# Kernel optimization log

Hardware: AMD Instinct MI355X
Metric: run time of the kernel (lower is better)

## Reference

```python
import jax, jax.numpy as jnp
import numpy as np

IMG = 128; P = 16; ND = IMG // P; N = ND * ND  # 64 patches
INF = 3 * P * P      # 768 flattened patch features
ATT = 768; HID = 3072; OUT = 768; B = 64
EPS = 1e-5


def setup_inputs() -> dict:
    key = jax.random.key(0)
    ks = jax.random.split(key, 24)
    w = lambda k, shape: jax.random.normal(k, shape, jnp.float32) * 0.02
    return {
        "x": jax.random.normal(ks[0], (B, 3, IMG, IMG), jnp.float32),
        # per-patch q/k/v projections: [n, in, out] weights, [n, out] biases
        "Wq": w(ks[1], (N, INF, ATT)), "bq": w(ks[2], (N, ATT)),
        "Wk": w(ks[3], (N, INF, ATT)), "bk": w(ks[4], (N, ATT)),
        "Wv": w(ks[5], (N, INF, ATT)), "bv": w(ks[6], (N, ATT)),
        "ln_g": jnp.ones((ATT,), jnp.float32), "ln_b": jnp.zeros((ATT,), jnp.float32),
        "p1_w": w(ks[7], (INF, ATT)), "p1_b": w(ks[8], (ATT,)),
        "w0": w(ks[9], (ATT, HID)),  "b0": w(ks[10], (HID,)),
        "w1": w(ks[11], (HID, HID)), "b1": w(ks[12], (HID,)),
        "w2": w(ks[13], (HID, HID)), "b2": w(ks[14], (HID,)),
        "w3": w(ks[15], (HID, HID)), "b3": w(ks[16], (HID,)),
        "w4": w(ks[17], (HID, OUT)), "b4": w(ks[18], (OUT,)),
        "p2_w": w(ks[19], (ATT, OUT)), "p2_b": w(ks[20], (OUT,)),
    }


def _forward(x, Wq, bq, Wk, bk, Wv, bv, ln_g, ln_b, p1_w, p1_b,
             w0, b0, w1, b1, w2, b2, w3, b3, w4, b4, p2_w, p2_b):
    b_ = x.shape[0]
    # patch split (row-major over (i,j) blocks) then flatten channel*patch dims
    flat = x.reshape(b_, 3, ND, P, ND, P).transpose(0, 2, 4, 1, 3, 5).reshape(b_, N, INF)
    # per-patch projections, attention taken ACROSS the batch dim (as in source)
    q = jnp.einsum('bnf,nfd->bnd', flat, Wq) + bq
    k = jnp.einsum('bnf,nfd->bnd', flat, Wk) + bk
    v = jnp.einsum('bnf,nfd->bnd', flat, Wv) + bv
    scores = jnp.einsum('bnd,cnd->nbc', q, k) / jnp.sqrt(jnp.float32(ATT))  # [n,B,B]
    attn = jnp.einsum('nbc,cnd->bnd', jax.nn.softmax(scores, axis=-1), v)  # [B,n,ATT]
    # LayerNorm(att_features)
    mu = attn.mean(-1, keepdims=True)
    var = ((attn - mu) ** 2).mean(-1, keepdims=True)
    ln = (attn - mu) / jnp.sqrt(var + EPS) * ln_g + ln_b
    att = ln + flat @ p1_w + p1_b
    # linear stack (no nonlinearity in the source)
    h = att @ w0 + b0
    h = h @ w1 + b1
    h = h @ w2 + b2
    h = h @ w3 + b3
    h = h @ w4 + b4
    proj = h + att @ p2_w + p2_b
    return jax.nn.softmax(proj, axis=2)


def reference(x, Wq, bq, Wk, bk, Wv, bv, ln_g, ln_b, p1_w, p1_b,
              w0, b0, w1, b1, w2, b2, w3, b3, w4, b4, p2_w, p2_b):
    return _forward(x, Wq, bq, Wk, bk, Wv, bv, ln_g, ln_b, p1_w, p1_b,
                    w0, b0, w1, b1, w2, b2, w3, b3, w4, b4, p2_w, p2_b)
```

## Files before the change

kernel.cpp:

```cpp
#include <hip/hip_runtime.h>
#include <hip/hip_bf16.h>

using bf16 = __bf16;
using bf16x8 = __bf16 __attribute__((ext_vector_type(8)));
using f32x4 = float __attribute__((ext_vector_type(4)));

static constexpr long ROWEL = 64L * 768;

__device__ __forceinline__ void async16(void* lds, const void* g)
{
    __builtin_amdgcn_global_load_lds((const __attribute__((address_space(1))) void*)g,
                                     (__attribute__((address_space(3))) void*)lds, 16, 0, 0);
}

__global__ __launch_bounds__(256) void k_patchify(const float* __restrict__ x, bf16* __restrict__ flat)
{
    const int n = blockIdx.x;
    const int b = blockIdx.y;
    const int i_ = n >> 3, j_ = n & 7;
    for (int it = 0; it < 3; ++it) {
        int f = threadIdx.x + it * 256;
        int c = f >> 8, rem = f & 255, pi = rem >> 4, pj = rem & 15;
        float v = x[(((long)(b * 3 + c)) << 14) + ((i_ * 16 + pi) << 7) + (j_ * 16 + pj)];
        flat[(long)b * ROWEL + n * 768 + f] = (bf16)v;
    }
}

__global__ __launch_bounds__(256) void k_cvt_t(const float* __restrict__ W, bf16* __restrict__ Wt,
                                               int Kd, int Nd)
{
    __shared__ bf16 T[64 * 66];
    const int k0 = blockIdx.x * 64, n0 = blockIdx.y * 64;
    const int tid = threadIdx.x;
    const int kr = tid >> 4, nc = (tid & 15) * 4;
#pragma unroll
    for (int i = 0; i < 4; ++i) {
        f32x4 v = *(const f32x4*)(W + (long)(k0 + kr + i * 16) * Nd + n0 + nc);
#pragma unroll
        for (int e = 0; e < 4; ++e)
            T[(kr + i * 16) * 66 + nc + e] = (bf16)v[e];
    }
    __syncthreads();
    const int nr = tid >> 3, ks = (tid & 7) * 8;
#pragma unroll
    for (int it = 0; it < 2; ++it) {
        int n = nr + it * 32;
        bf16x8 o;
#pragma unroll
        for (int j = 0; j < 8; ++j) o[j] = T[(ks + j) * 66 + n];
        *(bf16x8*)(Wt + (long)(n0 + n) * Kd + k0 + ks) = o;
    }
}

__global__ __launch_bounds__(256) void k_cast(const float* __restrict__ W, bf16* __restrict__ o, long nelem)
{
    long i = ((long)blockIdx.x * 256 + threadIdx.x) * 8;
    if (i >= nelem) return;
    f32x4 a = *(const f32x4*)(W + i);
    f32x4 b = *(const f32x4*)(W + i + 4);
    bf16x8 v;
#pragma unroll
    for (int e = 0; e < 4; ++e) { v[e] = (bf16)a[e]; v[4 + e] = (bf16)b[e]; }
    *(bf16x8*)(o + i) = v;
}

template<int BM, int BN>
__global__ __launch_bounds__(256) void k_gemm_bt(
    const bf16* __restrict__ A, long lda,
    const bf16* __restrict__ Bt, long ldb,
    int K,
    const float* __restrict__ bias,
    const float* __restrict__ addm,
    bf16* __restrict__ Cb, float* __restrict__ Cf, long ldc)
{
    constexpr int WM = BM / 2, WN = BN / 2, FM = WM / 16, FN = WN / 16;
    __shared__ bf16 As[BM * 32];
    __shared__ bf16 Bs[BN * 32];
    const int tid = threadIdx.x, lane = tid & 63, wave = tid >> 6;
    const int wm = wave >> 1, wn = wave & 1;
    const long m0 = (long)blockIdx.x * BM, n0 = (long)blockIdx.y * BN;

    f32x4 acc[FM][FN];
#pragma unroll
    for (int i = 0; i < FM; ++i)
#pragma unroll
        for (int j = 0; j < FN; ++j) acc[i][j] = (f32x4){0.f, 0.f, 0.f, 0.f};

    const int nk = K >> 5;
    for (int kt = 0; kt < nk; ++kt) {
        const long kb = (long)kt * 32;
#pragma unroll
        for (int i = 0; i < BM / 64; ++i) {
            const int idx = tid + i * 256;
            const int r = idx >> 2, seg = idx & 3;
            async16(&As[(i * 256 + wave * 64) * 8], A + (m0 + r) * lda + kb + seg * 8);
        }
#pragma unroll
        for (int i = 0; i < BN / 64; ++i) {
            const int idx = tid + i * 256;
            const int r = idx >> 2, seg = idx & 3;
            async16(&Bs[(i * 256 + wave * 64) * 8], Bt + (n0 + r) * ldb + kb + seg * 8);
        }
        __syncthreads();
        bf16x8 af[FM], bfr[FN];
#pragma unroll
        for (int i = 0; i < FM; ++i)
            af[i] = *(const bf16x8*)&As[(wm * WM + i * 16 + (lane & 15)) * 32 + (lane >> 4) * 8];
#pragma unroll
        for (int j = 0; j < FN; ++j)
            bfr[j] = *(const bf16x8*)&Bs[(wn * WN + j * 16 + (lane & 15)) * 32 + (lane >> 4) * 8];
#pragma unroll
        for (int i = 0; i < FM; ++i)
#pragma unroll
            for (int j = 0; j < FN; ++j)
                acc[i][j] = __builtin_amdgcn_mfma_f32_16x16x32_bf16(af[i], bfr[j], acc[i][j], 0, 0, 0);
        __syncthreads();
    }

#pragma unroll
    for (int j = 0; j < FN; ++j) {
        const long col = n0 + wn * WN + j * 16 + (lane & 15);
        const float bb = bias ? bias[col] : 0.f;
#pragma unroll
        for (int i = 0; i < FM; ++i) {
#pragma unroll
            for (int r = 0; r < 4; ++r) {
                const long row = m0 + wm * WM + i * 16 + (lane >> 4) * 4 + r;
                const long idx = row * ldc + col;
                float v = acc[i][j][r] + bb;
                if (addm) v += addm[idx];
                if (Cb) Cb[idx] = (bf16)v;
                if (Cf) Cf[idx] = v;
            }
        }
    }
}

__global__ __launch_bounds__(256) void k_qkv(
    const bf16* __restrict__ flat, const float* __restrict__ W, const float* __restrict__ bias,
    bf16* __restrict__ out)
{
    __shared__ bf16 As[64 * 32];
    __shared__ float Bs[32 * 64];
    const int tid = threadIdx.x, lane = tid & 63, wave = tid >> 6;
    const int wm = wave >> 1, wn = wave & 1;
    const int n0 = blockIdx.x * 64;
    const int z = blockIdx.y;
    const float* Wz = W + (long)z * 589824;

    f32x4 acc[2][2];
#pragma unroll
    for (int i = 0; i < 2; ++i)
#pragma unroll
        for (int j = 0; j < 2; ++j) acc[i][j] = (f32x4){0.f, 0.f, 0.f, 0.f};

    for (int kt = 0; kt < 24; ++kt) {
        const int kb = kt * 32;
        {
            const int r = tid >> 2, seg = tid & 3;
            async16(&As[wave * 512], flat + (long)r * ROWEL + z * 768 + kb + seg * 8);
        }
#pragma unroll
        for (int i = 0; i < 2; ++i) {
            const int g = i * 4 + wave;
            const int kk = kb + g * 4 + (lane >> 4);
            const int nn = (lane & 15) * 4;
            async16(&Bs[g * 256], Wz + (long)kk * 768 + n0 + nn);
        }
        __syncthreads();
        bf16x8 af[2], bfr[2];
#pragma unroll
        for (int i = 0; i < 2; ++i)
            af[i] = *(const bf16x8*)&As[(wm * 32 + i * 16 + (lane & 15)) * 32 + (lane >> 4) * 8];
#pragma unroll
        for (int j = 0; j < 2; ++j) {
            const int n = wn * 32 + j * 16 + (lane & 15);
            const int kf = (lane >> 4) * 8;
            bf16x8 b;
#pragma unroll
            for (int e = 0; e < 8; ++e) b[e] = (bf16)Bs[(kf + e) * 64 + n];
            bfr[j] = b;
        }
#pragma unroll
        for (int i = 0; i < 2; ++i)
#pragma unroll
            for (int j = 0; j < 2; ++j)
                acc[i][j] = __builtin_amdgcn_mfma_f32_16x16x32_bf16(af[i], bfr[j], acc[i][j], 0, 0, 0);
        __syncthreads();
    }

#pragma unroll
    for (int j = 0; j < 2; ++j) {
        const int col = n0 + wn * 32 + j * 16 + (lane & 15);
        const float bb = bias[z * 768 + col];
#pragma unroll
        for (int i = 0; i < 2; ++i) {
#pragma unroll
            for (int r = 0; r < 4; ++r) {
                const int row = wm * 32 + i * 16 + (lane >> 4) * 4 + r;
                out[(long)row * ROWEL + z * 768 + col] = (bf16)(acc[i][j][r] + bb);
            }
        }
    }
}

__global__ __launch_bounds__(256) void k_vm(
    const float* __restrict__ vin, const float* __restrict__ W,
    int K, int N, float* __restrict__ outP)
{
    __shared__ float red[4][64];
    const int tid = threadIdx.x;
    const int nl = tid & 63, kq = tid >> 6;
    const int n = blockIdx.x * 64 + nl;
    const int kc = blockIdx.y;
    const int kchunk = K / 8, kslice = kchunk / 4;
    const int k0 = kc * kchunk + kq * kslice;
    float acc = 0.f;
#pragma unroll 8
    for (int k = k0; k < k0 + kslice; ++k)
        acc += vin[k] * W[(long)k * N + n];
    red[kq][nl] = acc;
    __syncthreads();
    if (kq == 0)
        outP[(long)kc * N + n] = red[0][nl] + red[1][nl] + red[2][nl] + red[3][nl];
}

__global__ __launch_bounds__(256) void k_vred(
    const float* __restrict__ P, const float* __restrict__ b1, const float* __restrict__ b2,
    int N, float* __restrict__ out)
{
    const int n = blockIdx.x * 256 + threadIdx.x;
    if (n >= N) return;
    float s = b1[n] + (b2 ? b2[n] : 0.f);
#pragma unroll
    for (int j = 0; j < 8; ++j) s += P[(long)j * N + n];
    out[n] = s;
}

__global__ __launch_bounds__(256) void k_madd(const float* __restrict__ MTf, const float* __restrict__ p2w,
                                              bf16* __restrict__ Mt)
{
    const int n = blockIdx.x;
    for (int k = threadIdx.x; k < 768; k += 256)
        Mt[n * 768 + k] = (bf16)(MTf[n * 768 + k] + p2w[(long)k * 768 + n]);
}

__global__ __launch_bounds__(256) void k_attn(
    const bf16* __restrict__ q, const bf16* __restrict__ k, const bf16* __restrict__ v,
    float* __restrict__ attn)
{
    const int n = blockIdx.x;
    __shared__ bf16 QT[64 * 72];
    __shared__ bf16 KT[64 * 72];
    __shared__ float S[64 * 66];
    __shared__ bf16 P[64 * 72];
    __shared__ bf16 VT[128 * 72];

    const int tid = threadIdx.x, lane = tid & 63, wave = tid >> 6;
    const int wm = wave >> 1, wn = wave & 1;

    f32x4 accs[2][2];
#pragma unroll
    for (int i = 0; i < 2; ++i)
#pragma unroll
        for (int j = 0; j < 2; ++j) accs[i][j] = (f32x4){0.f, 0.f, 0.f, 0.f};

    for (int kt = 0; kt < 12; ++kt) {
#pragma unroll
        for (int i = 0; i < 2; ++i) {
            int cid = tid + i * 256;
            int r = cid >> 3, seg = cid & 7;
            *(bf16x8*)&QT[r * 72 + seg * 8] = *(const bf16x8*)(q + (long)r * ROWEL + n * 768 + kt * 64 + seg * 8);
            *(bf16x8*)&KT[r * 72 + seg * 8] = *(const bf16x8*)(k + (long)r * ROWEL + n * 768 + kt * 64 + seg * 8);
        }
        __syncthreads();
#pragma unroll
        for (int ks = 0; ks < 2; ++ks) {
            bf16x8 qa[2], kb[2];
#pragma unroll
            for (int i = 0; i < 2; ++i)
                qa[i] = *(const bf16x8*)&QT[(wm * 32 + i * 16 + (lane & 15)) * 72 + ks * 32 + (lane >> 4) * 8];
#pragma unroll
            for (int j = 0; j < 2; ++j)
                kb[j] = *(const bf16x8*)&KT[(wn * 32 + j * 16 + (lane & 15)) * 72 + ks * 32 + (lane >> 4) * 8];
#pragma unroll
            for (int i = 0; i < 2; ++i)
#pragma unroll
                for (int j = 0; j < 2; ++j)
                    accs[i][j] = __builtin_amdgcn_mfma_f32_16x16x32_bf16(qa[i], kb[j], accs[i][j], 0, 0, 0);
        }
        __syncthreads();
    }
    const float sc = 0.03608439182435161f;
#pragma unroll
    for (int i = 0; i < 2; ++i)
#pragma unroll
        for (int j = 0; j < 2; ++j)
#pragma unroll
            for (int r = 0; r < 4; ++r)
                S[(wm * 32 + i * 16 + (lane >> 4) * 4 + r) * 66 + wn * 32 + j * 16 + (lane & 15)] = accs[i][j][r] * sc;
    __syncthreads();

    {
        int r = tid >> 2, l4 = tid & 3;
        float m = -1e30f;
        for (int c = l4; c < 64; c += 4) m = fmaxf(m, S[r * 66 + c]);
        m = fmaxf(m, __shfl_xor(m, 1));
        m = fmaxf(m, __shfl_xor(m, 2));
        float s = 0.f;
        for (int c = l4; c < 64; c += 4) { float e = __expf(S[r * 66 + c] - m); S[r * 66 + c] = e; s += e; }
        s += __shfl_xor(s, 1);
        s += __shfl_xor(s, 2);
        float inv = 1.f / s;
        for (int c = l4; c < 64; c += 4) P[r * 72 + c] = (bf16)(S[r * 66 + c] * inv);
    }
    __syncthreads();

    for (int dc = 0; dc < 6; ++dc) {
#pragma unroll
        for (int i = 0; i < 4; ++i) {
            int cid = tid + i * 256;
            int c = cid >> 4, seg = cid & 15;
            bf16x8 vv = *(const bf16x8*)(v + (long)c * ROWEL + n * 768 + dc * 128 + seg * 8);
#pragma unroll
            for (int e = 0; e < 8; ++e)
                VT[(seg * 8 + e) * 72 + c] = vv[e];
        }
        __syncthreads();
        f32x4 acco[2][4];
#pragma unroll
        for (int i = 0; i < 2; ++i)
#pragma unroll
            for (int j = 0; j < 4; ++j) acco[i][j] = (f32x4){0.f, 0.f, 0.f, 0.f};
#pragma unroll
        for (int ks = 0; ks < 2; ++ks) {
            bf16x8 pa[2], vb[4];
#pragma unroll
            for (int i = 0; i < 2; ++i)
                pa[i] = *(const bf16x8*)&P[(wm * 32 + i * 16 + (lane & 15)) * 72 + ks * 32 + (lane >> 4) * 8];
#pragma unroll
            for (int j = 0; j < 4; ++j)
                vb[j] = *(const bf16x8*)&VT[(wn * 64 + j * 16 + (lane & 15)) * 72 + ks * 32 + (lane >> 4) * 8];
#pragma unroll
            for (int i = 0; i < 2; ++i)
#pragma unroll
                for (int j = 0; j < 4; ++j)
                    acco[i][j] = __builtin_amdgcn_mfma_f32_16x16x32_bf16(pa[i], vb[j], acco[i][j], 0, 0, 0);
        }
#pragma unroll
        for (int i = 0; i < 2; ++i)
#pragma unroll
            for (int j = 0; j < 4; ++j)
#pragma unroll
                for (int r = 0; r < 4; ++r) {
                    long b = wm * 32 + i * 16 + (lane >> 4) * 4 + r;
                    int d = dc * 128 + wn * 64 + j * 16 + (lane & 15);
                    attn[b * ROWEL + n * 768 + d] = acco[i][j][r];
                }
        __syncthreads();
    }
}

__global__ __launch_bounds__(256) void k_ln(float* __restrict__ a,
                                            const float* __restrict__ g, const float* __restrict__ bb)
{
    const long row = blockIdx.x * 4 + (threadIdx.x >> 6);
    const int lane = threadIdx.x & 63;
    float* p = a + row * 768;
    f32x4 xv[3];
    float s = 0.f;
#pragma unroll
    for (int c = 0; c < 3; ++c) {
        xv[c] = *(const f32x4*)(p + c * 256 + lane * 4);
        s += xv[c][0] + xv[c][1] + xv[c][2] + xv[c][3];
    }
#pragma unroll
    for (int o = 1; o < 64; o <<= 1) s += __shfl_xor(s, o);
    const float mu = s * (1.f / 768.f);
    float vs = 0.f;
#pragma unroll
    for (int c = 0; c < 3; ++c)
#pragma unroll
        for (int e = 0; e < 4; ++e) { float d = xv[c][e] - mu; vs += d * d; }
#pragma unroll
    for (int o = 1; o < 64; o <<= 1) vs += __shfl_xor(vs, o);
    const float rstd = rsqrtf(vs * (1.f / 768.f) + 1e-5f);
#pragma unroll
    for (int c = 0; c < 3; ++c)
#pragma unroll
        for (int e = 0; e < 4; ++e) {
            int col = c * 256 + lane * 4 + e;
            p[col] = (xv[c][e] - mu) * rstd * g[col] + bb[col];
        }
}

__global__ __launch_bounds__(256) void k_softmax(float* __restrict__ o)
{
    const long row = blockIdx.x * 4 + (threadIdx.x >> 6);
    const int lane = threadIdx.x & 63;
    float* p = o + row * 768;
    f32x4 xv[3];
    float m = -1e30f;
#pragma unroll
    for (int c = 0; c < 3; ++c) {
        xv[c] = *(const f32x4*)(p + c * 256 + lane * 4);
        m = fmaxf(m, fmaxf(fmaxf(xv[c][0], xv[c][1]), fmaxf(xv[c][2], xv[c][3])));
    }
#pragma unroll
    for (int o2 = 1; o2 < 64; o2 <<= 1) m = fmaxf(m, __shfl_xor(m, o2));
    float s = 0.f;
#pragma unroll
    for (int c = 0; c < 3; ++c)
#pragma unroll
        for (int e = 0; e < 4; ++e) { float ev = __expf(xv[c][e] - m); xv[c][e] = ev; s += ev; }
#pragma unroll
    for (int o2 = 1; o2 < 64; o2 <<= 1) s += __shfl_xor(s, o2);
    const float inv = 1.f / s;
#pragma unroll
    for (int c = 0; c < 3; ++c)
        *(f32x4*)(p + c * 256 + lane * 4) = xv[c] * inv;
}

extern "C" void kernel_launch(void* const* d_in, const int* in_sizes, int n_in,
                              void* d_out, int out_size, void* d_ws, size_t ws_size,
                              hipStream_t stream)
{
    const float* x   = (const float*)d_in[0];
    const float* Wq  = (const float*)d_in[1];
    const float* bq  = (const float*)d_in[2];
    const float* Wk  = (const float*)d_in[3];
    const float* bk  = (const float*)d_in[4];
    const float* Wv  = (const float*)d_in[5];
    const float* bv  = (const float*)d_in[6];
    const float* lng = (const float*)d_in[7];
    const float* lnb = (const float*)d_in[8];
    const float* p1w = (const float*)d_in[9];
    const float* p1b = (const float*)d_in[10];
    const float* w0  = (const float*)d_in[11];
    const float* b0  = (const float*)d_in[12];
    const float* w1  = (const float*)d_in[13];
    const float* b1  = (const float*)d_in[14];
    const float* w2  = (const float*)d_in[15];
    const float* b2  = (const float*)d_in[16];
    const float* w3  = (const float*)d_in[17];
    const float* b3  = (const float*)d_in[18];
    const float* w4  = (const float*)d_in[19];
    const float* b4  = (const float*)d_in[20];
    const float* p2w = (const float*)d_in[21];
    const float* p2b = (const float*)d_in[22];
    float* out = (float*)d_out;

    char* wsbase = (char*)d_ws;
    size_t off = 0;
    auto alloc = [&](size_t bytes) { char* p = wsbase + off; off += (bytes + 255) & ~(size_t)255; return p; };
    bf16*  flat = (bf16*)alloc(4096L * 768 * 2);
    bf16*  qb   = (bf16*)alloc(4096L * 768 * 2);
    bf16*  kb   = (bf16*)alloc(4096L * 768 * 2);
    bf16*  vb2  = (bf16*)alloc(4096L * 768 * 2);
    float* attn = (float*)alloc(4096L * 768 * 4);
    bf16*  att  = (bf16*)alloc(4096L * 768 * 2);
    bf16*  p1t  = (bf16*)alloc(768L * 768 * 2);
    bf16*  w0c  = (bf16*)alloc(768L * 3072 * 2);
    bf16*  w1c  = (bf16*)alloc(3072L * 3072 * 2);
    bf16*  w2c  = (bf16*)alloc(3072L * 3072 * 2);
    bf16*  w3c  = (bf16*)alloc(3072L * 3072 * 2);
    bf16*  w4t  = (bf16*)alloc(768L * 3072 * 2);
    bf16*  M1   = (bf16*)alloc(768L * 3072 * 2);
    bf16*  M2   = (bf16*)alloc(768L * 3072 * 2);
    float* MTf  = (float*)alloc(768L * 768 * 4);
    bf16*  Mt   = (bf16*)alloc(768L * 768 * 2);
    float* vP   = (float*)alloc(8L * 3072 * 4);
    float* c1   = (float*)alloc(3072 * 4);
    float* c2   = (float*)alloc(3072 * 4);
    float* c3   = (float*)alloc(3072 * 4);
    float* c4   = (float*)alloc(768 * 4);
    if (off > ws_size) return;

    k_patchify<<<dim3(64, 64), 256, 0, stream>>>(x, flat);
    k_qkv<<<dim3(12, 64), 256, 0, stream>>>(flat, Wq, bq, qb);
    k_qkv<<<dim3(12, 64), 256, 0, stream>>>(flat, Wk, bk, kb);
    k_qkv<<<dim3(12, 64), 256, 0, stream>>>(flat, Wv, bv, vb2);
    k_attn<<<64, 256, 0, stream>>>(qb, kb, vb2, attn);
    k_ln<<<1024, 256, 0, stream>>>(attn, lng, lnb);
    k_cvt_t<<<dim3(12, 12), 256, 0, stream>>>(p1w, p1t, 768, 768);
    k_gemm_bt<64, 128><<<dim3(64, 6), 256, 0, stream>>>(flat, 768, p1t, 768, 768, p1b, attn, att, nullptr, 768);

    k_cvt_t<<<dim3(48, 12), 256, 0, stream>>>(w4, w4t, 3072, 768);
    k_cast<<<4608, 256, 0, stream>>>(w1, w1c, 3072L * 3072);
    k_cast<<<4608, 256, 0, stream>>>(w2, w2c, 3072L * 3072);
    k_cast<<<4608, 256, 0, stream>>>(w3, w3c, 3072L * 3072);
    k_cast<<<1152, 256, 0, stream>>>(w0, w0c, 768L * 3072);

    k_gemm_bt<64, 128><<<dim3(12, 24), 256, 0, stream>>>(w4t, 3072, w3c, 3072, 3072, nullptr, nullptr, M1, nullptr, 3072);
    k_gemm_bt<64, 128><<<dim3(12, 24), 256, 0, stream>>>(M1, 3072, w2c, 3072, 3072, nullptr, nullptr, M2, nullptr, 3072);
    k_gemm_bt<64, 128><<<dim3(12, 24), 256, 0, stream>>>(M2, 3072, w1c, 3072, 3072, nullptr, nullptr, M1, nullptr, 3072);
    k_gemm_bt<64, 64><<<dim3(12, 12), 256, 0, stream>>>(M1, 3072, w0c, 3072, 3072, nullptr, nullptr, nullptr, MTf, 768);
    k_madd<<<768, 256, 0, stream>>>(MTf, p2w, Mt);

    k_vm<<<dim3(48, 8), 256, 0, stream>>>(b0, w1, 3072, 3072, vP);
    k_vred<<<12, 256, 0, stream>>>(vP, b1, nullptr, 3072, c1);
    k_vm<<<dim3(48, 8), 256, 0, stream>>>(c1, w2, 3072, 3072, vP);
    k_vred<<<12, 256, 0, stream>>>(vP, b2, nullptr, 3072, c2);
    k_vm<<<dim3(48, 8), 256, 0, stream>>>(c2, w3, 3072, 3072, vP);
    k_vred<<<12, 256, 0, stream>>>(vP, b3, nullptr, 3072, c3);
    k_vm<<<dim3(12, 8), 256, 0, stream>>>(c3, w4, 3072, 768, vP);
    k_vred<<<3, 256, 0, stream>>>(vP, b4, p2b, 768, c4);

    k_gemm_bt<64, 128><<<dim3(64, 6), 256, 0, stream>>>(att, 768, Mt, 768, 768, c4, nullptr, nullptr, out, 768);
    k_softmax<<<1024, 256, 0, stream>>>(out);
}
```

Baseline: 509.9 us.

## Double-buffer GEMM staging, fuse weight casts into GEMM, fold vred into vm

```diff
diff --git a/kernel.cpp b/kernel.cpp
--- a/kernel.cpp
+++ b/kernel.cpp
@@ -52,18 +52,6 @@
     }
 }
 
-__global__ __launch_bounds__(256) void k_cast(const float* __restrict__ W, bf16* __restrict__ o, long nelem)
-{
-    long i = ((long)blockIdx.x * 256 + threadIdx.x) * 8;
-    if (i >= nelem) return;
-    f32x4 a = *(const f32x4*)(W + i);
-    f32x4 b = *(const f32x4*)(W + i + 4);
-    bf16x8 v;
-#pragma unroll
-    for (int e = 0; e < 4; ++e) { v[e] = (bf16)a[e]; v[4 + e] = (bf16)b[e]; }
-    *(bf16x8*)(o + i) = v;
-}
-
 template<int BM, int BN>
 __global__ __launch_bounds__(256) void k_gemm_bt(
     const bf16* __restrict__ A, long lda,
@@ -74,8 +62,8 @@
     bf16* __restrict__ Cb, float* __restrict__ Cf, long ldc)
 {
     constexpr int WM = BM / 2, WN = BN / 2, FM = WM / 16, FN = WN / 16;
-    __shared__ bf16 As[BM * 32];
-    __shared__ bf16 Bs[BN * 32];
+    __shared__ bf16 As[2][BM * 32];
+    __shared__ bf16 Bs[2][BN * 32];
     const int tid = threadIdx.x, lane = tid & 63, wave = tid >> 6;
     const int wm = wave >> 1, wn = wave & 1;
     const long m0 = (long)blockIdx.x * BM, n0 = (long)blockIdx.y * BN;
@@ -87,34 +75,42 @@
         for (int j = 0; j < FN; ++j) acc[i][j] = (f32x4){0.f, 0.f, 0.f, 0.f};
 
     const int nk = K >> 5;
+
+    auto stage = [&](int buf, int kt) {
+        const long kb = (long)kt * 32;
+#pragma unroll
+        for (int i = 0; i < BM / 64; ++i) {
+            const int c = i * 256 + tid;
+            const int r = c >> 2, seg = c & 3;
+            async16(&As[buf][(i * 256 + wave * 64) * 8], A + (m0 + r) * lda + kb + seg * 8);
+        }
+#pragma unroll
+        for (int i = 0; i < BN / 64; ++i) {
+            const int c = i * 256 + tid;
+            const int r = c >> 2, seg = c & 3;
+            async16(&Bs[buf][(i * 256 + wave * 64) * 8], Bt + (n0 + r) * ldb + kb + seg * 8);
+        }
+    };
+
+    stage(0, 0);
+    __syncthreads();
+    int cur = 0;
     for (int kt = 0; kt < nk; ++kt) {
-        const long kb = (long)kt * 32;
-#pragma unroll
-        for (int i = 0; i < BM / 64; ++i) {
-            const int idx = tid + i * 256;
-            const int r = idx >> 2, seg = idx & 3;
-            async16(&As[(i * 256 + wave * 64) * 8], A + (m0 + r) * lda + kb + seg * 8);
-        }
-#pragma unroll
-        for (int i = 0; i < BN / 64; ++i) {
-            const int idx = tid + i * 256;
-            const int r = idx >> 2, seg = idx & 3;
-            async16(&Bs[(i * 256 + wave * 64) * 8], Bt + (n0 + r) * ldb + kb + seg * 8);
-        }
-        __syncthreads();
+        if (kt + 1 < nk) stage(cur ^ 1, kt + 1);
         bf16x8 af[FM], bfr[FN];
 #pragma unroll
         for (int i = 0; i < FM; ++i)
-            af[i] = *(const bf16x8*)&As[(wm * WM + i * 16 + (lane & 15)) * 32 + (lane >> 4) * 8];
+            af[i] = *(const bf16x8*)&As[cur][(wm * WM + i * 16 + (lane & 15)) * 32 + (lane >> 4) * 8];
 #pragma unroll
         for (int j = 0; j < FN; ++j)
-            bfr[j] = *(const bf16x8*)&Bs[(wn * WN + j * 16 + (lane & 15)) * 32 + (lane >> 4) * 8];
+            bfr[j] = *(const bf16x8*)&Bs[cur][(wn * WN + j * 16 + (lane & 15)) * 32 + (lane >> 4) * 8];
 #pragma unroll
         for (int i = 0; i < FM; ++i)
 #pragma unroll
             for (int j = 0; j < FN; ++j)
                 acc[i][j] = __builtin_amdgcn_mfma_f32_16x16x32_bf16(af[i], bfr[j], acc[i][j], 0, 0, 0);
         __syncthreads();
+        cur ^= 1;
     }
 
 #pragma unroll
@@ -136,12 +132,91 @@
     }
 }
 
+__global__ __launch_bounds__(256) void k_gemm_f32b(
+    const bf16* __restrict__ A, long lda,
+    const float* __restrict__ Bf, long ldb,
+    int K,
+    bf16* __restrict__ Cb, float* __restrict__ Cf, long ldc)
+{
+    __shared__ bf16 As[2][64 * 32];
+    __shared__ float Bs[2][128 * 32];
+    const int tid = threadIdx.x, lane = tid & 63, wave = tid >> 6;
+    const int wm = wave >> 1, wn = wave & 1;
+    const long m0 = (long)blockIdx.x * 64, n0 = (long)blockIdx.y * 128;
+
+    f32x4 acc[2][4];
+#pragma unroll
+    for (int i = 0; i < 2; ++i)
+#pragma unroll
+        for (int j = 0; j < 4; ++j) acc[i][j] = (f32x4){0.f, 0.f, 0.f, 0.f};
+
+    const int nk = K >> 5;
+
+    auto stage = [&](int buf, int kt) {
+        const long kb = (long)kt * 32;
+        {
+            const int r = tid >> 2, seg = tid & 3;
+            async16(&As[buf][wave * 64 * 8], A + (m0 + r) * lda + kb + seg * 8);
+        }
+#pragma unroll
+        for (int it = 0; it < 4; ++it) {
+            const int c = it * 256 + tid;
+            const int n = c >> 3, sg = (c & 7) ^ (n & 7);
+            async16(&Bs[buf][(it * 256 + wave * 64) * 4], Bf + (n0 + n) * ldb + kb + sg * 4);
+        }
+    };
+
+    stage(0, 0);
+    __syncthreads();
+    int cur = 0;
+    for (int kt = 0; kt < nk; ++kt) {
+        if (kt + 1 < nk) stage(cur ^ 1, kt + 1);
+        bf16x8 af[2], bfr[4];
+#pragma unroll
+        for (int i = 0; i < 2; ++i)
+            af[i] = *(const bf16x8*)&As[cur][(wm * 32 + i * 16 + (lane & 15)) * 32 + (lane >> 4) * 8];
+#pragma unroll
+        for (int j = 0; j < 4; ++j) {
+            const int nn = wn * 64 + j * 16 + (lane & 15);
+            const int cs = nn & 7, s0 = (lane >> 4) * 2;
+            f32x4 lo = *(const f32x4*)&Bs[cur][nn * 32 + ((s0 ^ cs) << 2)];
+            f32x4 hi = *(const f32x4*)&Bs[cur][nn * 32 + (((s0 + 1) ^ cs) << 2)];
+            bf16x8 b;
+#pragma unroll
+            for (int e = 0; e < 4; ++e) { b[e] = (bf16)lo[e]; b[4 + e] = (bf16)hi[e]; }
+            bfr[j] = b;
+        }
+#pragma unroll
+        for (int i = 0; i < 2; ++i)
+#pragma unroll
+            for (int j = 0; j < 4; ++j)
+                acc[i][j] = __builtin_amdgcn_mfma_f32_16x16x32_bf16(af[i], bfr[j], acc[i][j], 0, 0, 0);
+        __syncthreads();
+        cur ^= 1;
+    }
+
+#pragma unroll
+    for (int j = 0; j < 4; ++j) {
+        const long col = n0 + wn * 64 + j * 16 + (lane & 15);
+#pragma unroll
+        for (int i = 0; i < 2; ++i) {
+#pragma unroll
+            for (int r = 0; r < 4; ++r) {
+                const long row = m0 + wm * 32 + i * 16 + (lane >> 4) * 4 + r;
+                const long idx = row * ldc + col;
+                if (Cb) Cb[idx] = (bf16)acc[i][j][r];
+                if (Cf) Cf[idx] = acc[i][j][r];
+            }
+        }
+    }
+}
+
 __global__ __launch_bounds__(256) void k_qkv(
     const bf16* __restrict__ flat, const float* __restrict__ W, const float* __restrict__ bias,
     bf16* __restrict__ out)
 {
-    __shared__ bf16 As[64 * 32];
-    __shared__ float Bs[32 * 64];
+    __shared__ bf16 As[2][64 * 32];
+    __shared__ float Bs[2][32 * 64];
     const int tid = threadIdx.x, lane = tid & 63, wave = tid >> 6;
     const int wm = wave >> 1, wn = wave & 1;
     const int n0 = blockIdx.x * 64;
@@ -154,31 +229,36 @@
 #pragma unroll
         for (int j = 0; j < 2; ++j) acc[i][j] = (f32x4){0.f, 0.f, 0.f, 0.f};
 
-    for (int kt = 0; kt < 24; ++kt) {
+    auto stage = [&](int buf, int kt) {
         const int kb = kt * 32;
         {
             const int r = tid >> 2, seg = tid & 3;
-            async16(&As[wave * 512], flat + (long)r * ROWEL + z * 768 + kb + seg * 8);
+            async16(&As[buf][wave * 512], flat + (long)r * ROWEL + z * 768 + kb + seg * 8);
         }
 #pragma unroll
         for (int i = 0; i < 2; ++i) {
-            const int g = i * 4 + wave;
-            const int kk = kb + g * 4 + (lane >> 4);
-            const int nn = (lane & 15) * 4;
-            async16(&Bs[g * 256], Wz + (long)kk * 768 + n0 + nn);
-        }
-        __syncthreads();
+            const int c = i * 256 + tid;
+            const int kl = c >> 4, nn = (c & 15) * 4;
+            async16(&Bs[buf][(i * 256 + wave * 64) * 4], Wz + (long)(kb + kl) * 768 + n0 + nn);
+        }
+    };
+
+    stage(0, 0);
+    __syncthreads();
+    int cur = 0;
+    for (int kt = 0; kt < 24; ++kt) {
+        if (kt + 1 < 24) stage(cur ^ 1, kt + 1);
         bf16x8 af[2], bfr[2];
 #pragma unroll
         for (int i = 0; i < 2; ++i)
-            af[i] = *(const bf16x8*)&As[(wm * 32 + i * 16 + (lane & 15)) * 32 + (lane >> 4) * 8];
+            af[i] = *(const bf16x8*)&As[cur][(wm * 32 + i * 16 + (lane & 15)) * 32 + (lane >> 4) * 8];
 #pragma unroll
         for (int j = 0; j < 2; ++j) {
             const int n = wn * 32 + j * 16 + (lane & 15);
             const int kf = (lane >> 4) * 8;
             bf16x8 b;
 #pragma unroll
-            for (int e = 0; e < 8; ++e) b[e] = (bf16)Bs[(kf + e) * 64 + n];
+            for (int e = 0; e < 8; ++e) b[e] = (bf16)Bs[cur][(kf + e) * 64 + n];
             bfr[j] = b;
         }
 #pragma unroll
@@ -187,6 +267,7 @@
             for (int j = 0; j < 2; ++j)
                 acc[i][j] = __builtin_amdgcn_mfma_f32_16x16x32_bf16(af[i], bfr[j], acc[i][j], 0, 0, 0);
         __syncthreads();
+        cur ^= 1;
     }
 
 #pragma unroll
@@ -204,9 +285,9 @@
     }
 }
 
-__global__ __launch_bounds__(256) void k_vm(
-    const float* __restrict__ vin, const float* __restrict__ W,
-    int K, int N, float* __restrict__ outP)
+__global__ __launch_bounds__(256) void k_vm2(
+    const float* __restrict__ Pin, const float* __restrict__ bin, const float* __restrict__ W,
+    int K, int N, float* __restrict__ Pout)
 {
     __shared__ float red[4][64];
     const int tid = threadIdx.x;
@@ -216,13 +297,19 @@
     const int kchunk = K / 8, kslice = kchunk / 4;
     const int k0 = kc * kchunk + kq * kslice;
     float acc = 0.f;
-#pragma unroll 8
-    for (int k = k0; k < k0 + kslice; ++k)
-        acc += vin[k] * W[(long)k * N + n];
+#pragma unroll 4
+    for (int k = k0; k < k0 + kslice; ++k) {
+        float vk = bin[k];
+        if (Pin) {
+#pragma unroll
+            for (int j = 0; j < 8; ++j) vk += Pin[(long)j * K + k];
+        }
+        acc += vk * W[(long)k * N + n];
+    }
     red[kq][nl] = acc;
     __syncthreads();
     if (kq == 0)
-        outP[(long)kc * N + n] = red[0][nl] + red[1][nl] + red[2][nl] + red[3][nl];
+        Pout[(long)kc * N + n] = red[0][nl] + red[1][nl] + red[2][nl] + red[3][nl];
 }
 
 __global__ __launch_bounds__(256) void k_vred(
@@ -460,19 +547,14 @@
     float* attn = (float*)alloc(4096L * 768 * 4);
     bf16*  att  = (bf16*)alloc(4096L * 768 * 2);
     bf16*  p1t  = (bf16*)alloc(768L * 768 * 2);
-    bf16*  w0c  = (bf16*)alloc(768L * 3072 * 2);
-    bf16*  w1c  = (bf16*)alloc(3072L * 3072 * 2);
-    bf16*  w2c  = (bf16*)alloc(3072L * 3072 * 2);
-    bf16*  w3c  = (bf16*)alloc(3072L * 3072 * 2);
     bf16*  w4t  = (bf16*)alloc(768L * 3072 * 2);
     bf16*  M1   = (bf16*)alloc(768L * 3072 * 2);
     bf16*  M2   = (bf16*)alloc(768L * 3072 * 2);
+    bf16*  M3   = (bf16*)alloc(768L * 3072 * 2);
     float* MTf  = (float*)alloc(768L * 768 * 4);
     bf16*  Mt   = (bf16*)alloc(768L * 768 * 2);
-    float* vP   = (float*)alloc(8L * 3072 * 4);
-    float* c1   = (float*)alloc(3072 * 4);
-    float* c2   = (float*)alloc(3072 * 4);
-    float* c3   = (float*)alloc(3072 * 4);
+    float* vPa  = (float*)alloc(8L * 3072 * 4);
+    float* vPb  = (float*)alloc(8L * 3072 * 4);
     float* c4   = (float*)alloc(768 * 4);
     if (off > ws_size) return;
 
@@ -486,25 +568,17 @@
     k_gemm_bt<64, 128><<<dim3(64, 6), 256, 0, stream>>>(flat, 768, p1t, 768, 768, p1b, attn, att, nullptr, 768);
 
     k_cvt_t<<<dim3(48, 12), 256, 0, stream>>>(w4, w4t, 3072, 768);
-    k_cast<<<4608, 256, 0, stream>>>(w1, w1c, 3072L * 3072);
-    k_cast<<<4608, 256, 0, stream>>>(w2, w2c, 3072L * 3072);
-    k_cast<<<4608, 256, 0, stream>>>(w3, w3c, 3072L * 3072);
-    k_cast<<<1152, 256, 0, stream>>>(w0, w0c, 768L * 3072);
-
-    k_gemm_bt<64, 128><<<dim3(12, 24), 256, 0, stream>>>(w4t, 3072, w3c, 3072, 3072, nullptr, nullptr, M1, nullptr, 3072);
-    k_gemm_bt<64, 128><<<dim3(12, 24), 256, 0, stream>>>(M1, 3072, w2c, 3072, 3072, nullptr, nullptr, M2, nullptr, 3072);
-    k_gemm_bt<64, 128><<<dim3(12, 24), 256, 0, stream>>>(M2, 3072, w1c, 3072, 3072, nullptr, nullptr, M1, nullptr, 3072);
-    k_gemm_bt<64, 64><<<dim3(12, 12), 256, 0, stream>>>(M1, 3072, w0c, 3072, 3072, nullptr, nullptr, nullptr, MTf, 768);
+    k_gemm_f32b<<<dim3(12, 24), 256, 0, stream>>>(w4t, 3072, w3, 3072, 3072, M1, nullptr, 3072);
+    k_gemm_f32b<<<dim3(12, 24), 256, 0, stream>>>(M1, 3072, w2, 3072, 3072, M2, nullptr, 3072);
+    k_gemm_f32b<<<dim3(12, 24), 256, 0, stream>>>(M2, 3072, w1, 3072, 3072, M3, nullptr, 3072);
+    k_gemm_f32b<<<dim3(12, 6),  256, 0, stream>>>(M3, 3072, w0, 3072, 3072, nullptr, MTf, 768);
     k_madd<<<768, 256, 0, stream>>>(MTf, p2w, Mt);
 
-    k_vm<<<dim3(48, 8), 256, 0, stream>>>(b0, w1, 3072, 3072, vP);
-    k_vred<<<12, 256, 0, stream>>>(vP, b1, nullptr, 3072, c1);
-    k_vm<<<dim3(48, 8), 256, 0, stream>>>(c1, w2, 3072, 3072, vP);
-    k_vred<<<12, 256, 0, stream>>>(vP, b2, nullptr, 3072, c2);
-    k_vm<<<dim3(48, 8), 256, 0, stream>>>(c2, w3, 3072, 3072, vP);
-    k_vred<<<12, 256, 0, stream>>>(vP, b3, nullptr, 3072, c3);
-    k_vm<<<dim3(12, 8), 256, 0, stream>>>(c3, w4, 3072, 768, vP);
-    k_vred<<<3, 256, 0, stream>>>(vP, b4, p2b, 768, c4);
+    k_vm2<<<dim3(48, 8), 256, 0, stream>>>(nullptr, b0, w1, 3072, 3072, vPa);
+    k_vm2<<<dim3(48, 8), 256, 0, stream>>>(vPa, b1, w2, 3072, 3072, vPb);
+    k_vm2<<<dim3(48, 8), 256, 0, stream>>>(vPb, b2, w3, 3072, 3072, vPa);
+    k_vm2<<<dim3(12, 8), 256, 0, stream>>>(vPa, b3, w4, 3072, 768, vPb);
+    k_vred<<<3, 256, 0, stream>>>(vPb, b4, p2b, 768, c4);
 
     k_gemm_bt<64, 128><<<dim3(64, 6), 256, 0, stream>>>(att, 768, Mt, 768, 768, c4, nullptr, nullptr, out, 768);
     k_softmax<<<1024, 256, 0, stream>>>(out);
```

Result: slower. 729.3 us (+43.0%).
